# Kernel optimization log

Measured on AMD Instinct MI355X. Metric: run time of the kernel, lower is better.

## Reference

```python
import jax, jax.numpy as jnp
import numpy as np

D_MODEL = 2048
N_HEADS = 16
D_HEAD = 128
ROPE_THETA = 10000.0


def _rope(x, offset):
    # x: [B, H, S, D]; half-rotation RoPE with position offset
    B, H, S, D = x.shape
    inv_freq = 1.0 / (ROPE_THETA ** (jnp.arange(0, D, 2, dtype=jnp.float32) / D))  # [D/2]
    pos = (offset + jnp.arange(S, dtype=jnp.float32))                              # [S]
    ang = pos[:, None] * inv_freq[None, :]                                         # [S, D/2]
    cos = jnp.cos(ang).astype(x.dtype)
    sin = jnp.sin(ang).astype(x.dtype)
    x1, x2 = x[..., : D // 2], x[..., D // 2 :]
    return jnp.concatenate([x1 * cos - x2 * sin, x2 * cos + x1 * sin], axis=-1)


def setup_inputs() -> dict:
    key = jax.random.key(0)
    ks = jax.random.split(key, 5)
    B, Sq, Skv = 4, 1024, 1024
    x = jax.random.normal(ks[0], (B, Sq, D_MODEL), dtype=jnp.float32)
    cache_k = jax.random.normal(ks[1], (B, N_HEADS, Skv, D_HEAD), dtype=jnp.float32)
    cache_v = jax.random.normal(ks[2], (B, N_HEADS, Skv, D_HEAD), dtype=jnp.float32)
    w_qkv = jax.random.normal(ks[3], (D_MODEL, 3 * D_MODEL), dtype=jnp.float32) * (D_MODEL ** -0.5)
    w_o = jax.random.normal(ks[4], (D_MODEL, D_MODEL), dtype=jnp.float32) * (D_MODEL ** -0.5)
    return {"x": x, "cache_k": cache_k, "cache_v": cache_v, "w_qkv": w_qkv, "w_o": w_o}


def reference(x, cache_k, cache_v, w_qkv, w_o):
    B, S, _ = x.shape
    offset = cache_k.shape[2]
    # fused QKV projection: [B, S, 3*d_model] -> [B, H, S, 3*d_head]
    qkv = jnp.einsum("bsd,de->bse", x, w_qkv)
    qkv = qkv.reshape(B, S, N_HEADS, 3 * D_HEAD).transpose(0, 2, 1, 3)
    q, k, v = jnp.split(qkv, 3, axis=-1)
    q = _rope(q, offset)
    k = _rope(k, offset)
    # KV-cache concat along sequence dim
    k = jnp.concatenate([cache_k, k], axis=2)  # [B, H, Skv+S, D]
    v = jnp.concatenate([cache_v, v], axis=2)
    # SDPA (no mask, matching mask=None path)
    scale = D_HEAD ** -0.5
    scores = jnp.einsum("bhqd,bhkd->bhqk", q, k) * scale
    attn = jax.nn.softmax(scores, axis=-1)
    out = jnp.einsum("bhqk,bhkd->bhqd", attn, v)           # [B, H, S, D]
    out = out.transpose(0, 2, 1, 3).reshape(B, S, D_MODEL)
    return jnp.einsum("bsd,de->bse", out, w_o)
```

## Files before the change

### kernel.cpp

```cpp
#include <hip/hip_runtime.h>


typedef __bf16 bf16x8 __attribute__((ext_vector_type(8)));
typedef float f32x4 __attribute__((ext_vector_type(4)));
typedef unsigned short u16x8 __attribute__((ext_vector_type(8)));
typedef unsigned short u16x4 __attribute__((ext_vector_type(4)));

__device__ __forceinline__ float b2f(unsigned short u) {
  return __builtin_bit_cast(float, (unsigned int)u << 16);
}
__device__ __forceinline__ unsigned short f2b(float f) {
  unsigned int x = __builtin_bit_cast(unsigned int, f);
  x += 0x7fffu + ((x >> 16) & 1u);
  return (unsigned short)(x >> 16);
}
__device__ __forceinline__ unsigned int cvt_pk_bf16(float lo, float hi) {
  unsigned int r;
  asm("v_cvt_pk_bf16_f32 %0, %1, %2" : "=v"(r) : "v"(lo), "v"(hi));
  return r;
}
__device__ __forceinline__ void gload_lds16(const void* g, void* l) {
  __builtin_amdgcn_global_load_lds(
      (__attribute__((address_space(1))) void*)(g),
      (__attribute__((address_space(3))) void*)(l), 16, 0, 0);
}
__device__ __forceinline__ void barrier_nodrain() {
  asm volatile("" ::: "memory");
  __builtin_amdgcn_s_barrier();
  asm volatile("" ::: "memory");
}

__global__ void build_trig(float* __restrict__ cs, float* __restrict__ sn) {
  int idx = blockIdx.x * 256 + threadIdx.x;
  int s = idx >> 6, i = idx & 63;
  float inv = exp2f(-(float)i * (13.287712379549449f / 64.0f));
  float ang = (float)(1024 + s) * inv;
  cs[idx] = cosf(ang);
  sn[idx] = sinf(ang);
}

__global__ void conv_bf16(const float* __restrict__ in, unsigned short* __restrict__ out) {
  size_t i = ((size_t)blockIdx.x * 256 + threadIdx.x) * 8;
  float4 a = *(const float4*)(in + i);
  float4 b = *(const float4*)(in + i + 4);
  u16x8 v;
  v[0] = f2b(a.x); v[1] = f2b(a.y); v[2] = f2b(a.z); v[3] = f2b(a.w);
  v[4] = f2b(b.x); v[5] = f2b(b.y); v[6] = f2b(b.z); v[7] = f2b(b.w);
  *(u16x8*)(out + i) = v;
}

__global__ __launch_bounds__(256) void transpose_conv(
    const float* __restrict__ in, unsigned short* __restrict__ out, int R, int C) {
  __shared__ float tile[32][33];
  int c0 = blockIdx.x * 32, r0 = blockIdx.y * 32;
  int tx = threadIdx.x & 31, ty = threadIdx.x >> 5;
#pragma unroll
  for (int j = 0; j < 4; ++j)
    tile[ty + j * 8][tx] = in[(size_t)(r0 + ty + j * 8) * C + c0 + tx];
  __syncthreads();
#pragma unroll
  for (int j = 0; j < 4; ++j)
    out[(size_t)(c0 + ty + j * 8) * R + r0 + tx] = f2b(tile[tx][ty + j * 8]);
}

__global__ void copy_k(const float* __restrict__ ck, unsigned short* __restrict__ Kf) {
  size_t idx = ((size_t)blockIdx.x * 256 + threadIdx.x) * 4;
  size_t bh = idx >> 17, rem = idx & 131071;
  float4 a = *(const float4*)(ck + idx);
  u16x4 v;
  v[0] = f2b(a.x); v[1] = f2b(a.y); v[2] = f2b(a.z); v[3] = f2b(a.w);
  *(u16x4*)(Kf + bh * 262144 + rem) = v;
}

__global__ __launch_bounds__(256) void rope_qk(
    const unsigned short* __restrict__ qkv, const float* __restrict__ cs,
    const float* __restrict__ sn, unsigned short* __restrict__ Qb,
    unsigned short* __restrict__ Kf) {
  int row = blockIdx.x;
  int b = row >> 10, s = row & 1023;
#pragma unroll
  for (int it = 0; it < 4; ++it) {
    int item = it * 256 + threadIdx.x;
    int h = item >> 6, i = item & 63;
    const unsigned short* base = qkv + (size_t)row * 6144 + h * 384;
    float q1 = b2f(base[i]),       q2 = b2f(base[64 + i]);
    float k1 = b2f(base[128 + i]), k2 = b2f(base[192 + i]);
    float c = cs[s * 64 + i], sv = sn[s * 64 + i];
    const float scale = 0.12751738f;
    size_t bh = (size_t)(b * 16 + h);
    unsigned short* qd = Qb + (bh * 1024 + s) * 128;
    qd[i]      = f2b((q1 * c - q2 * sv) * scale);
    qd[64 + i] = f2b((q2 * c + q1 * sv) * scale);
    unsigned short* kd = Kf + (bh * 2048 + 1024 + s) * 128;
    kd[i]      = f2b(k1 * c - k2 * sv);
    kd[64 + i] = f2b(k2 * c + k1 * sv);
  }
}

__global__ __launch_bounds__(256) void build_vt(
    const float* __restrict__ cv, const unsigned short* __restrict__ qkv,
    unsigned short* __restrict__ Vt) {
  __shared__ float tile[32][33];
  int bhid = blockIdx.z;
  int s0 = blockIdx.x * 32, d0 = blockIdx.y * 32;
  int tx = threadIdx.x & 31, ty = threadIdx.x >> 5;
  int b = bhid >> 4, h = bhid & 15;
#pragma unroll
  for (int j = 0; j < 4; ++j) {
    int s = s0 + ty + j * 8, d = d0 + tx;
    float v;
    if (s < 1024) v = cv[((size_t)bhid * 1024 + s) * 128 + d];
    else v = b2f(qkv[((size_t)b * 1024 + (s - 1024)) * 6144 + h * 384 + 256 + d]);
    tile[ty + j * 8][tx] = v;
  }
  __syncthreads();
#pragma unroll
  for (int j = 0; j < 4; ++j) {
    int d = d0 + ty + j * 8, s = s0 + tx;
    Vt[((size_t)bhid * 128 + d) * 2048 + s] = f2b(tile[tx][ty + j * 8]);
  }
}

template <int M, int N, int K, bool OUT_BF16>
__global__ __launch_bounds__(512, 4) void gemm_ring(
    const unsigned short* __restrict__ A, const unsigned short* __restrict__ B,
    void* __restrict__ Cout) {
  __shared__ __align__(16) char lds[3 * 24576];
  constexpr int NT = N / 128;
  constexpr int Kt = K / 32;
  int bid = blockIdx.x;
  int tm = bid / NT, tn = bid % NT;
  int tid = threadIdx.x;
  int lane = tid & 63, wave = tid >> 6;
  int wr = (wave >> 1) * 64, wc = (wave & 1) * 64;
  int l15 = lane & 15, g = lane >> 4;

  int p = tid * 16;
  const unsigned short* aSrc0 = A + (size_t)(tm * 256 + (p >> 6)) * K + ((p & 63) >> 1);
  const unsigned short* aSrc1 = aSrc0 + (size_t)128 * K;
  const unsigned short* bSrc  = B + (size_t)(tn * 128 + (p >> 6)) * K + ((p & 63) >> 1);

  f32x4 acc[4][4] = {};

  auto stage = [&](int s) {
    char* base = (char*)lds + s * 24576;
    gload_lds16(aSrc0, base + p);
    gload_lds16(aSrc1, base + 8192 + p);
    gload_lds16(bSrc,  base + 16384 + p);
    aSrc0 += 32; aSrc1 += 32; bSrc += 32;
  };

  stage(0);
  stage(1);
  asm volatile("s_waitcnt vmcnt(3)" ::: "memory");

  int slot = 0, sNext = 2;
  for (int t = 0; t < Kt; ++t) {
    barrier_nodrain();
    if (t + 2 < Kt) {
      stage(sNext);
      sNext = (sNext == 2) ? 0 : sNext + 1;
      asm volatile("s_waitcnt vmcnt(3)" ::: "memory");
    } else {
      asm volatile("s_waitcnt vmcnt(0)" ::: "memory");
    }
    const char* As_ = (const char*)lds + slot * 24576;
    const char* Bs_ = As_ + 16384;
    bf16x8 af[4], bfr[4];
#pragma unroll
    for (int m = 0; m < 4; ++m)
      af[m] = *(const bf16x8*)(As_ + (wr + m * 16 + l15) * 64 + g * 16);
#pragma unroll
    for (int n = 0; n < 4; ++n)
      bfr[n] = *(const bf16x8*)(Bs_ + (wc + n * 16 + l15) * 64 + g * 16);
    __builtin_amdgcn_s_setprio(1);
#pragma unroll
    for (int m = 0; m < 4; ++m)
#pragma unroll
      for (int n = 0; n < 4; ++n)
        acc[m][n] = __builtin_amdgcn_mfma_f32_16x16x32_bf16(af[m], bfr[n], acc[m][n], 0, 0, 0);
    __builtin_amdgcn_s_setprio(0);
    slot = (slot == 2) ? 0 : slot + 1;
  }

#pragma unroll
  for (int m = 0; m < 4; ++m) {
    int row0 = tm * 256 + wr + m * 16 + g * 4;
#pragma unroll
    for (int n = 0; n < 4; ++n) {
      int col = tn * 128 + wc + n * 16 + l15;
#pragma unroll
      for (int r = 0; r < 4; ++r) {
        size_t off = (size_t)(row0 + r) * N + col;
        if constexpr (OUT_BF16) ((unsigned short*)Cout)[off] = f2b(acc[m][n][r]);
        else ((float*)Cout)[off] = acc[m][n][r];
      }
    }
  }
}

__global__ __launch_bounds__(256, 4) void attn_kernel(
    const unsigned short* __restrict__ Qb,
    const unsigned short* __restrict__ Kf,
    const unsigned short* __restrict__ Vt,
    unsigned short* __restrict__ Out) {
  __shared__ __align__(16) unsigned short Ks[64 * 128];
  __shared__ __align__(16) unsigned short Vs[128 * 64];
  __shared__ __align__(16) char PsRaw[4 * 2048];

  int bid = blockIdx.x;
  bid = (bid & 7) * 128 + (bid >> 3);
  int bh = bid >> 4, qt = bid & 15;
  int tid = threadIdx.x, lane = tid & 63, wave = tid >> 6;
  int l15 = lane & 15, g = lane >> 4;
  int swz = (l15 & 7) << 4;

  bf16x8 qf[4];
  const unsigned short* qp = Qb + ((size_t)(bh * 1024 + qt * 64 + wave * 16 + l15)) * 128;
#pragma unroll
  for (int kk = 0; kk < 4; ++kk)
    qf[kk] = *(const bf16x8*)(qp + kk * 32 + g * 8);

  const unsigned short* Kbase = Kf + (size_t)bh * 2048 * 128;
  const unsigned short* Vbase = Vt + (size_t)bh * 128 * 2048;
  const unsigned short* kptr[4];
  const unsigned short* vptr[4];
  char* kdst[4];
  char* vdst[4];
#pragma unroll
  for (int is = 0; is < 4; ++is) {
    int p = tid * 16 + is * 4096;
    int lgk = p ^ (((p >> 8) & 7) << 4);
    kptr[is] = Kbase + (size_t)(lgk >> 8) * 128 + ((lgk & 255) >> 1);
    kdst[is] = (char*)Ks + is * 4096 + (tid & 192) * 16;
    int lgv = p ^ (((p >> 7) & 7) << 4);
    vptr[is] = Vbase + (size_t)(lgv >> 7) * 2048 + ((lgv & 127) >> 1);
    vdst[is] = (char*)Vs + is * 4096 + (tid & 192) * 16;
  }
  char* ps = PsRaw + wave * 2048 + l15 * 128;
  const char* ksA = (const char*)Ks + l15 * 256;
  const char* vsA = (const char*)Vs + l15 * 128;

  float mrun = -1e30f, lsum = 0.f;
  f32x4 acc[8] = {};

  for (int it = 0; it < 32; ++it) {
#pragma unroll
    for (int is = 0; is < 4; ++is) {
      gload_lds16(kptr[is], kdst[is]);  kptr[is] += 64 * 128;
      gload_lds16(vptr[is], vdst[is]);  vptr[is] += 64;
    }
    __syncthreads();

    f32x4 st[4] = {};
#pragma unroll
    for (int kk = 0; kk < 4; ++kk) {
#pragma unroll
      for (int t = 0; t < 4; ++t) {
        bf16x8 a = *(const bf16x8*)(ksA + t * 4096 + ((kk * 64 + g * 16) ^ swz));
        st[t] = __builtin_amdgcn_mfma_f32_16x16x32_bf16(a, qf[kk], st[t], 0, 0, 0);
      }
    }

    float m0 = fmaxf(fmaxf(st[0][0], st[0][1]), st[0][2]);
    float m1 = fmaxf(fmaxf(st[0][3], st[1][0]), st[1][1]);
    float m2 = fmaxf(fmaxf(st[1][2], st[1][3]), st[2][0]);
    float m3 = fmaxf(fmaxf(st[2][1], st[2][2]), st[2][3]);
    float m4 = fmaxf(fmaxf(st[3][0], st[3][1]), st[3][2]);
    float pmax = fmaxf(fmaxf(fmaxf(m0, m1), fmaxf(m2, m3)), fmaxf(m4, st[3][3]));
    pmax = fmaxf(pmax, __shfl_xor(pmax, 16));
    pmax = fmaxf(pmax, __shfl_xor(pmax, 32));

    if (!__all(pmax - mrun <= 8.0f)) {
      float mnew = fmaxf(mrun, pmax);
      float corr = exp2f(mrun - mnew);
      lsum *= corr;
#pragma unroll
      for (int mt = 0; mt < 8; ++mt) acc[mt] *= corr;
      mrun = mnew;
    }

    float psA = 0.f, psB = 0.f;
    float pv[4][4];
#pragma unroll
    for (int t = 0; t < 4; ++t) {
      pv[t][0] = exp2f(st[t][0] - mrun);
      pv[t][1] = exp2f(st[t][1] - mrun);
      pv[t][2] = exp2f(st[t][2] - mrun);
      pv[t][3] = exp2f(st[t][3] - mrun);
      psA += pv[t][0] + pv[t][1];
      psB += pv[t][2] + pv[t][3];
    }
    float psum = psA + psB;
    psum += __shfl_xor(psum, 16);
    psum += __shfl_xor(psum, 32);
    lsum += psum;

#pragma unroll
    for (int t = 0; t < 4; ++t) {
      uint2 w;
      w.x = cvt_pk_bf16(pv[t][0], pv[t][1]);
      w.y = cvt_pk_bf16(pv[t][2], pv[t][3]);
      *(uint2*)(ps + ((t * 32 + g * 8) ^ swz)) = w;
    }

#pragma unroll
    for (int k2 = 0; k2 < 2; ++k2) {
      bf16x8 pfr = *(const bf16x8*)(ps + ((k2 * 64 + g * 16) ^ swz));
#pragma unroll
      for (int mt = 0; mt < 8; ++mt) {
        bf16x8 a = *(const bf16x8*)(vsA + mt * 2048 + ((k2 * 64 + g * 16) ^ swz));
        acc[mt] = __builtin_amdgcn_mfma_f32_16x16x32_bf16(a, pfr, acc[mt], 0, 0, 0);
      }
    }
    __syncthreads();
  }

  float inv = 1.f / lsum;
  int b = bh >> 4, h = bh & 15;
  int sq = qt * 64 + wave * 16 + l15;
  unsigned short* orow = Out + ((size_t)(b * 1024 + sq) * 16 + h) * 128;
#pragma unroll
  for (int mt = 0; mt < 8; ++mt) {
    uint2 w;
    w.x = cvt_pk_bf16(acc[mt][0] * inv, acc[mt][1] * inv);
    w.y = cvt_pk_bf16(acc[mt][2] * inv, acc[mt][3] * inv);
    *(uint2*)(orow + mt * 16 + g * 4) = w;
  }
}

extern "C" void kernel_launch(void* const* d_in, const int* in_sizes, int n_in,
                              void* d_out, int out_size, void* d_ws, size_t ws_size,
                              hipStream_t stream) {
  const float* x       = (const float*)d_in[0];
  const float* cache_k = (const float*)d_in[1];
  const float* cache_v = (const float*)d_in[2];
  const float* w_qkv   = (const float*)d_in[3];
  const float* w_o     = (const float*)d_in[4];
  float* out = (float*)d_out;

  char* W = (char*)d_ws;
  constexpr size_t O_TRIG = 0;
  constexpr size_t O_XB   = 524288;
  constexpr size_t O_WQT  = O_XB  + 16777216;
  constexpr size_t O_WOT  = O_WQT + 25165824;
  constexpr size_t O_QKV  = O_WOT + 8388608;
  constexpr size_t O_QB   = O_QKV + 50331648;
  constexpr size_t O_KF   = O_QB  + 16777216;
  constexpr size_t O_VT   = O_KF  + 33554432;
  float* cs_tab = (float*)(W + O_TRIG);
  float* sn_tab = (float*)(W + O_TRIG + 262144);
  unsigned short* xb   = (unsigned short*)(W + O_XB);
  unsigned short* wqT  = (unsigned short*)(W + O_WQT);
  unsigned short* woT  = (unsigned short*)(W + O_WOT);
  unsigned short* qkv  = (unsigned short*)(W + O_QKV);
  unsigned short* qb   = (unsigned short*)(W + O_QB);
  unsigned short* Kf   = (unsigned short*)(W + O_KF);
  unsigned short* Vt   = (unsigned short*)(W + O_VT);
  unsigned short* attn_out = xb;

  build_trig<<<256, 256, 0, stream>>>(cs_tab, sn_tab);
  conv_bf16<<<4096, 256, 0, stream>>>(x, xb);
  transpose_conv<<<dim3(192, 64), 256, 0, stream>>>(w_qkv, wqT, 2048, 6144);
  transpose_conv<<<dim3(64, 64), 256, 0, stream>>>(w_o, woT, 2048, 2048);
  gemm_ring<4096, 6144, 2048, true><<<768, 512, 0, stream>>>(xb, wqT, qkv);
  rope_qk<<<4096, 256, 0, stream>>>(qkv, cs_tab, sn_tab, qb, Kf);
  copy_k<<<8192, 256, 0, stream>>>(cache_k, Kf);
  build_vt<<<dim3(64, 4, 64), 256, 0, stream>>>(cache_v, qkv, Vt);
  attn_kernel<<<1024, 256, 0, stream>>>(qb, Kf, Vt, attn_out);
  gemm_ring<4096, 2048, 2048, false><<<256, 512, 0, stream>>>(attn_out, woT, out);
}
```

Measured before the change: 361.3 us.

## Double-buffer K/V tiles in attention and compute row sums via MFMA

The attention kernel now keeps two LDS buffers for K and V and issues the next tile's global-to-LDS loads before computing on the current one. It waits on a partial vmcnt instead of fully draining at a barrier, so memory latency can overlap with compute. The softmax denominator is accumulated by an extra MFMA against a vector of ones, replacing the scalar adds and cross-lane shuffles. LDS use doubles and launch bounds drop to 2 blocks per CU, which lowers occupancy. The sum also now comes from bf16-rounded probabilities.

```diff
diff --git a/kernel.cpp b/kernel.cpp
--- a/kernel.cpp
+++ b/kernel.cpp
@@ -199,13 +199,13 @@
   }
 }
 
-__global__ __launch_bounds__(256, 4) void attn_kernel(
+__global__ __launch_bounds__(256, 2) void attn_kernel(
     const unsigned short* __restrict__ Qb,
     const unsigned short* __restrict__ Kf,
     const unsigned short* __restrict__ Vt,
     unsigned short* __restrict__ Out) {
-  __shared__ __align__(16) unsigned short Ks[64 * 128];
-  __shared__ __align__(16) unsigned short Vs[128 * 64];
+  __shared__ __align__(16) unsigned short Ks[2][64 * 128];
+  __shared__ __align__(16) unsigned short Vs[2][64 * 128];
   __shared__ __align__(16) char PsRaw[4 * 2048];
 
   int bid = blockIdx.x;
@@ -221,36 +221,54 @@
   for (int kk = 0; kk < 4; ++kk)
     qf[kk] = *(const bf16x8*)(qp + kk * 32 + g * 8);
 
+  u16x8 ou;
+#pragma unroll
+  for (int j = 0; j < 8; ++j) ou[j] = 0x3F80;
+  bf16x8 ones = __builtin_bit_cast(bf16x8, ou);
+
   const unsigned short* Kbase = Kf + (size_t)bh * 2048 * 128;
   const unsigned short* Vbase = Vt + (size_t)bh * 128 * 2048;
   const unsigned short* kptr[4];
   const unsigned short* vptr[4];
-  char* kdst[4];
-  char* vdst[4];
+  char* kdst0[4];
+  char* vdst0[4];
 #pragma unroll
   for (int is = 0; is < 4; ++is) {
     int p = tid * 16 + is * 4096;
     int lgk = p ^ (((p >> 8) & 7) << 4);
     kptr[is] = Kbase + (size_t)(lgk >> 8) * 128 + ((lgk & 255) >> 1);
-    kdst[is] = (char*)Ks + is * 4096 + (tid & 192) * 16;
+    kdst0[is] = (char*)Ks + is * 4096 + (tid & 192) * 16;
     int lgv = p ^ (((p >> 7) & 7) << 4);
     vptr[is] = Vbase + (size_t)(lgv >> 7) * 2048 + ((lgv & 127) >> 1);
-    vdst[is] = (char*)Vs + is * 4096 + (tid & 192) * 16;
+    vdst0[is] = (char*)Vs + is * 4096 + (tid & 192) * 16;
   }
   char* ps = PsRaw + wave * 2048 + l15 * 128;
-  const char* ksA = (const char*)Ks + l15 * 256;
-  const char* vsA = (const char*)Vs + l15 * 128;
-
-  float mrun = -1e30f, lsum = 0.f;
+
+  auto stage = [&](int buf) {
+#pragma unroll
+    for (int is = 0; is < 4; ++is) {
+      gload_lds16(kptr[is], kdst0[is] + buf * 16384);  kptr[is] += 64 * 128;
+      gload_lds16(vptr[is], vdst0[is] + buf * 16384);  vptr[is] += 64;
+    }
+  };
+
+  float mrun = -1e30f;
   f32x4 acc[8] = {};
-
+  f32x4 acc_l = {};
+
+  stage(0);
   for (int it = 0; it < 32; ++it) {
-#pragma unroll
-    for (int is = 0; is < 4; ++is) {
-      gload_lds16(kptr[is], kdst[is]);  kptr[is] += 64 * 128;
-      gload_lds16(vptr[is], vdst[is]);  vptr[is] += 64;
-    }
-    __syncthreads();
+    int cur = it & 1;
+    barrier_nodrain();
+    if (it + 1 < 32) {
+      stage(cur ^ 1);
+      asm volatile("s_waitcnt vmcnt(8)" ::: "memory");
+    } else {
+      asm volatile("s_waitcnt vmcnt(0)" ::: "memory");
+    }
+    barrier_nodrain();
+    const char* ksA = (const char*)Ks + cur * 16384 + l15 * 256;
+    const char* vsA = (const char*)Vs + cur * 16384 + l15 * 128;
 
     f32x4 st[4] = {};
 #pragma unroll
@@ -274,13 +292,12 @@
     if (!__all(pmax - mrun <= 8.0f)) {
       float mnew = fmaxf(mrun, pmax);
       float corr = exp2f(mrun - mnew);
-      lsum *= corr;
+      acc_l *= corr;
 #pragma unroll
       for (int mt = 0; mt < 8; ++mt) acc[mt] *= corr;
       mrun = mnew;
     }
 
-    float psA = 0.f, psB = 0.f;
     float pv[4][4];
 #pragma unroll
     for (int t = 0; t < 4; ++t) {
@@ -288,13 +305,7 @@
       pv[t][1] = exp2f(st[t][1] - mrun);
       pv[t][2] = exp2f(st[t][2] - mrun);
       pv[t][3] = exp2f(st[t][3] - mrun);
-      psA += pv[t][0] + pv[t][1];
-      psB += pv[t][2] + pv[t][3];
-    }
-    float psum = psA + psB;
-    psum += __shfl_xor(psum, 16);
-    psum += __shfl_xor(psum, 32);
-    lsum += psum;
+    }
 
 #pragma unroll
     for (int t = 0; t < 4; ++t) {
@@ -307,16 +318,16 @@
 #pragma unroll
     for (int k2 = 0; k2 < 2; ++k2) {
       bf16x8 pfr = *(const bf16x8*)(ps + ((k2 * 64 + g * 16) ^ swz));
+      acc_l = __builtin_amdgcn_mfma_f32_16x16x32_bf16(ones, pfr, acc_l, 0, 0, 0);
 #pragma unroll
       for (int mt = 0; mt < 8; ++mt) {
         bf16x8 a = *(const bf16x8*)(vsA + mt * 2048 + ((k2 * 64 + g * 16) ^ swz));
         acc[mt] = __builtin_amdgcn_mfma_f32_16x16x32_bf16(a, pfr, acc[mt], 0, 0, 0);
       }
     }
-    __syncthreads();
-  }
-
-  float inv = 1.f / lsum;
+  }
+
+  float inv = 1.f / acc_l[0];
   int b = bh >> 4, h = bh & 15;
   int sq = qt * 64 + wave * 16 + l15;
   unsigned short* orow = Out + ((size_t)(b * 1024 + sq) * 16 + h) * 128;
```

Measured after the change: 359.3 us. No clear change (-0.6%).
